# Kernel optimization log

Measured on AMD Instinct MI355X. Metric: run time of the kernel, lower is better.

## Reference

```python
import jax, jax.numpy as jnp
import numpy as np
from jax import lax

# Problem sizes (match input_specs)
N, D, M = 16384, 1024, 128
# GaussBAE hyperparameters: scl (init 1.0), alpha=sparse_reg, beta=tree_reg, temp
SCL, ALPHA, BETA, TEMP = 1.0, 0.1, 1.0, 0.5


def setup_inputs() -> dict:
    key = jax.random.key(0)
    k1, k2, k3 = jax.random.split(key, 3)
    X = jax.random.normal(k1, (N, D), jnp.float32)
    W = jax.random.normal(k2, (D, M), jnp.float32) / np.float32(np.sqrt(D))
    S0 = jax.random.randint(k3, (N, M), 0, 2).astype(jnp.int32)  # binary init states
    b = jnp.zeros((D,), jnp.float32)
    return {"X": X, "S0": S0, "W": W, "b": b}


def gibbs_sweep(X, S0, W):
    """Faithful JAX port of update_concepts_asym_cntr (one sweep, steps=1).

    Sequential over samples i (outer scan) and features j (inner scan),
    with rank-1 running updates of StS = S^T S and St1 = S^T 1.
    Deterministic ascending i/j order (original uses random permutations);
    Bernoulli uniforms are pre-drawn with a fixed key.
    """
    n, m = S0.shape
    S = S0.astype(jnp.float32)
    C = X @ W                                        # (n, m): X[i] @ W[:, j]
    U = jax.random.uniform(jax.random.key(1), (n, m), jnp.float32)
    StS = S.T @ S                                    # (m, m)
    St1 = S.sum(0)                                   # (m,)
    nf = jnp.float32(n)

    def outer_step(carry, xs):
        St1, StS = carry
        s_i, c_i, u_i = xs                           # (m,), (m,), (m,)
        # remove sample i from running stats
        St1 = St1 - s_i
        StS = StS - jnp.outer(s_i, s_i)
        # 2x2 contingency counts for each concept pair (m, m)
        D1 = StS
        D2 = St1[None, :] - StS
        D3 = St1[:, None] - StS
        D4 = nf - 1.0 - St1[None, :] - St1[:, None] + StS
        b1 = ((D1 < D2) & (D1 < D3) & (D1 < D4)).astype(jnp.float32)
        b2 = ((D2 < D1) & (D2 < D3) & (D2 < D4)).astype(jnp.float32)
        b3 = ((D3 < D2) & (D3 < D1) & (D3 < D4)).astype(jnp.float32)
        b4 = ((D4 < D2) & (D4 < D3) & (D4 < D1)).astype(jnp.float32)
        R = b1 - b2 - b3 + b4                        # (m, m)
        r = b2.sum(0) - b4.sum(0)                    # (m,)
        # centered input drive (constant over inner loop)
        inp = 2.0 * c_i - SCL * (nf - 1.0 - 2.0 * St1) / nf - ALPHA

        def inner_step(s, j):
            # tree-regularizer inhibition depends on current (partially updated) s
            inhib = R[j] @ s + r[j]
            prob = jax.nn.sigmoid((inp[j] - BETA * SCL * inhib) / TEMP)
            s = s.at[j].set((u_i[j] < prob).astype(jnp.float32))
            return s, None

        s_new, _ = lax.scan(inner_step, s_i, jnp.arange(m))
        # add updated sample i back to running stats
        St1 = St1 + s_new
        StS = StS + jnp.outer(s_new, s_new)
        return (St1, StS), s_new

    (_, _), S_new = lax.scan(outer_step, (St1, StS), (S, C, U))
    return S_new                                     # (n, m) in {0, 1}


def reference(X, S0, W, b):
    S_new = gibbs_sweep(X, S0, W)
    # GaussBAE.__call__: scl * S @ W.T + b
    out = SCL * (S_new @ W.T) + b
    return out
```

## Files before the change

### kernel.cpp

```cpp
#include <hip/hip_runtime.h>
#include <cmath>

typedef unsigned long long u64;
typedef unsigned int u32;

#define N_SAMP 16384
#define M_C 128

#define DEFER_ROW0 10240
#define DEFER_ROWS 192

__device__ __forceinline__ void tf2x32(u32 x0, u32 x1, u32& o0, u32& o1) {
  const u32 k0 = 0u, k1 = 1u;
  const u32 ks2 = k0 ^ k1 ^ 0x1BD11BDAu;
  x0 += k0; x1 += k1;
#define RND(r) { x0 += x1; x1 = (x1 << (r)) | (x1 >> (32 - (r))); x1 ^= x0; }
  RND(13) RND(15) RND(26) RND(6)  x0 += k1;  x1 += ks2 + 1u;
  RND(17) RND(29) RND(16) RND(24) x0 += ks2; x1 += k0 + 2u;
  RND(13) RND(15) RND(26) RND(6)  x0 += k0;  x1 += k1 + 3u;
  RND(17) RND(29) RND(16) RND(24) x0 += k1;  x1 += ks2 + 4u;
  RND(13) RND(15) RND(26) RND(6)  x0 += ks2; x1 += k0 + 5u;
#undef RND
  o0 = x0; o1 = x1;
}

__global__ void k_logit(float* __restrict__ Ub, double* __restrict__ Lgb) {
  int tid = blockIdx.x * 256 + threadIdx.x;
  if (tid >= N_SAMP * M_C) return;
  u32 o0, o1; tf2x32(0u, (u32)tid, o0, o1);
  u32 bits = o0 ^ o1;
  float u = __uint_as_float((bits >> 9) | 0x3f800000u) - 1.0f;
  Ub[tid] = u;
  double lg;
  if (u <= 0.0f) lg = -1e300;
  else { double ud = (double)u; lg = 0.5 * (log(ud) - log1p(-ud)); }
  Lgb[tid] = lg;
}

__global__ void k_pack(const int* __restrict__ S0, u64* __restrict__ S0m) {
  int row = blockIdx.x; int lane = threadIdx.x;
  int v0 = S0[row * 128 + lane];
  int v1 = S0[row * 128 + 64 + lane];
  u64 lo = __ballot(v0 != 0);
  u64 hi = __ballot(v1 != 0);
  if (lane == 0) { S0m[row * 2] = lo; S0m[row * 2 + 1] = hi; }
}

__global__ void k_colbits(const u64* __restrict__ S0m, u64* __restrict__ colb) {
  int wblk = blockIdx.x; int lane = threadIdx.x;
  int row = wblk * 64 + lane;
  u64 lo = S0m[row * 2], hi = S0m[row * 2 + 1];
  for (int cc = 0; cc < 64; ++cc) {
    u64 bal = __ballot((int)((lo >> cc) & 1ull));
    if (lane == 0) colb[cc * 256 + wblk] = bal;
  }
  for (int cc = 0; cc < 64; ++cc) {
    u64 bal = __ballot((int)((hi >> cc) & 1ull));
    if (lane == 0) colb[(64 + cc) * 256 + wblk] = bal;
  }
}

__global__ __launch_bounds__(256) void k_sts(const u64* __restrict__ colb, int* __restrict__ StSg) {
  int tid = blockIdx.x * 256 + threadIdx.x;
  int c = tid >> 7, k = tid & 127;
  int s = 0;
  for (int ww = 0; ww < 256; ++ww)
    s += __popcll(colb[c * 256 + ww] & colb[k * 256 + ww]);
  StSg[c * 128 + k] = s;
}

__global__ __launch_bounds__(256) void k_gemmC(const float* __restrict__ X,
                                               const float* __restrict__ W,
                                               double* __restrict__ Cb) {
  __shared__ float Xs[16][128];
  const int t = threadIdx.x;
  const int i0 = blockIdx.x * 16;
  const int j = t & 127;
  const int ih = t >> 7;
  double acc[8];
#pragma unroll
  for (int m = 0; m < 8; ++m) acc[m] = 0.0;
  for (int k0 = 0; k0 < 1024; k0 += 128) {
    __syncthreads();
#pragma unroll
    for (int m = 0; m < 8; ++m) {
      int e = t + 256 * m;
      int r = e >> 7, cc = e & 127;
      Xs[r][cc] = X[(i0 + r) * 1024 + k0 + cc];
    }
    __syncthreads();
#pragma unroll 4
    for (int kk = 0; kk < 128; ++kk) {
      double wd = (double)W[(k0 + kk) * 128 + j];
#pragma unroll
      for (int m = 0; m < 8; ++m)
        acc[m] += (double)Xs[ih * 8 + m][kk] * wd;
    }
  }
#pragma unroll
  for (int m = 0; m < 8; ++m)
    Cb[(i0 + ih * 8 + m) * 128 + j] = acc[m];
}

__global__ void k_wt(const float* __restrict__ W, float* __restrict__ Wt) {
  int d0 = blockIdx.x; int j = threadIdx.x;
  Wt[j * 1024 + d0] = W[d0 * 128 + j];
}

__device__ __forceinline__ bool condQ(double inpd, float uv, int hh) {
  double d = inpd - (double)hh;
  double pr = 1.0 / (1.0 + exp(-2.0 * d));
  return (double)uv < pr;
}

__device__ __forceinline__ int computeQ(double cv, float uv, double lg, int st1p) {
  double inp = 2.0 * cv - (16383.0 - 2.0 * (double)st1p) * (1.0 / 16384.0) - 0.1;
  if (uv <= 0.0f) return (1 << 20);
  double gd = floor(inp - lg);
  gd = fmin(fmax(gd, -300.0), 300.0);
  int h = (int)gd;
  if (condQ(inp, uv, h)) {
    if (condQ(inp, uv, h + 1)) { h++; if (condQ(inp, uv, h + 1)) h++; }
  } else {
    h--; if (!condQ(inp, uv, h)) h--;
  }
  return h;
}

__global__ __launch_bounds__(1024, 1) void k_gibbs(
    const double* __restrict__ Cb, const float* __restrict__ Ub,
    const double* __restrict__ Lgb, const u64* __restrict__ S0m,
    const int* __restrict__ StSg, u64* __restrict__ Som)
{
  __shared__ int RbufI[4096];
  __shared__ __align__(16) int St1s[128];
  __shared__ int redR[8][128];
  __shared__ int redP[8][128];
  __shared__ double cbuf[2][128];
  __shared__ float ubuf[2][128];
  __shared__ double lbuf[2][128];
  __shared__ int qbuf[128];
  __shared__ u32 simask[2][4];
  __shared__ u32 pnmask[4];
  __shared__ u32 pomask[4];

  const int t = threadIdx.x;
  const int lane = t & 63;
  const int w = t >> 6;
  const int c = t & 127;
  const int g = t >> 7;

  int sts[16];
#pragma unroll
  for (int m = 0; m < 16; ++m) sts[m] = StSg[c * 128 + g * 16 + m];

  if (t < 128) St1s[t] = StSg[t * 129];
  if (t < 4) { pnmask[t] = 0u; pomask[t] = 0u;
               simask[0][t] = (u32)(S0m[t >> 1] >> ((t & 1) * 32)); }
  if (w == 1) {
    cbuf[0][lane] = Cb[lane];            cbuf[0][64 + lane] = Cb[64 + lane];
    ubuf[0][lane] = Ub[lane];            ubuf[0][64 + lane] = Ub[64 + lane];
    lbuf[0][lane] = Lgb[lane];           lbuf[0][64 + lane] = Lgb[64 + lane];
  }
  __syncthreads();

#pragma unroll 1
  for (int i = 0; i < N_SAMP; ++i) {
    const int buf = i & 1;

    if (w == 1 && (i + 1) < N_SAMP) {
      const int nb = buf ^ 1;
      cbuf[nb][lane]      = Cb[(i + 1) * 128 + lane];
      cbuf[nb][64 + lane] = Cb[(i + 1) * 128 + 64 + lane];
      ubuf[nb][lane]      = Ub[(i + 1) * 128 + lane];
      ubuf[nb][64 + lane] = Ub[(i + 1) * 128 + 64 + lane];
      lbuf[nb][lane]      = Lgb[(i + 1) * 128 + lane];
      lbuf[nb][64 + lane] = Lgb[(i + 1) * 128 + 64 + lane];
      if (lane < 4)
        simask[nb][lane] = (u32)(S0m[(i + 1) * 2 + (lane >> 1)] >> ((lane & 1) * 32));
    }

    if (w == 2 || w == 3) {
      const int cc = t & 127;
      u32 sic = (simask[buf][cc >> 5] >> (cc & 31)) & 1u;
      int st1p = St1s[cc] - (int)sic;
      qbuf[cc] = computeQ(cbuf[buf][cc], ubuf[buf][cc], lbuf[buf][cc], st1p);
    }

    u32 PNw = (pnmask[g >> 1] >> ((g & 1) * 16)) & 0xffffu;
    u32 POw = (pomask[g >> 1] >> ((g & 1) * 16)) & 0xffffu;
    u32 SIw = (simask[buf][g >> 1] >> ((g & 1) * 16)) & 0xffffu;
    u32 pn_c = (pnmask[c >> 5] >> (c & 31)) & 1u;
    u32 po_c = (pomask[c >> 5] >> (c & 31)) & 1u;
    u32 si_c = (simask[buf][c >> 5] >> (c & 31)) & 1u;
    u32 Pw = pn_c ? PNw : 0u;
    u32 Mw = po_c ? POw : 0u;
    u32 Sw = si_c ? SIw : 0u;
    int p1 = St1s[c] - (int)si_c;
    int cpq = 16383 - p1;
    int racc = 0, pacc = 0;
#pragma unroll
    for (int ch = 0; ch < 4; ++ch) {
      int4 q4 = *(const int4*)&St1s[g * 16 + ch * 4];
      int qarr[4] = { q4.x, q4.y, q4.z, q4.w };
      u32 word = 0u;
#pragma unroll
      for (int e = 0; e < 4; ++e) {
        const int kk = ch * 4 + e;
        int a = sts[kk] + (int)((Pw >> kk) & 1u) - (int)((Mw >> kk) & 1u);
        sts[kk] = a;
        int sik = (int)((SIw >> kk) & 1u);
        int ap = a - (int)((Sw >> kk) & 1u);
        int q = qarr[e] - sik;
        int D2 = q - ap, D3 = p1 - ap, D4 = cpq - q + ap;
        int m14 = min(ap, D4), m23 = min(D2, D3);
        bool A = m14 < m23, B = m23 < m14;
        int R = (A && (ap != D4)) ? 1 : ((B && (D2 != D3)) ? -1 : 0);
        int b24 = (int)(B && (D3 < D2)) - (int)(A && (D4 < ap));
        racc += b24;
        pacc += R * sik;
        word |= ((u32)(R & 255)) << (8 * e);
      }
      RbufI[c * 32 + ((g * 4 + ch) ^ (c & 31))] = (int)word;
    }
    redR[g][c] = racc;
    redP[g][c] = pacc;
    __syncthreads();

    if (w == 0) {
      int rlo = 0, rhi = 0, plo = 0, phi = 0;
#pragma unroll
      for (int gg = 0; gg < 8; ++gg) {
        rlo += redR[gg][lane];       rhi += redR[gg][lane + 64];
        plo += redP[gg][lane];       phi += redP[gg][lane + 64];
      }
      u64 si_lo = (u64)simask[buf][0] | ((u64)simask[buf][1] << 32);
      u64 si_hi = (u64)simask[buf][2] | ((u64)simask[buf][3] << 32);
      int qlo = qbuf[lane] - rlo;
      int qhi = qbuf[lane + 64] - rhi;
      u64 nm_lo = 0ull, nm_hi = 0ull;
      const int rowL = lane * 32;
      const int rowH = (lane + 64) * 32;
      const int sw = lane & 31;

      int tl3[3], th3[3];
      tl3[0] = RbufI[rowL + (0 ^ sw)]; th3[0] = RbufI[rowH + (0 ^ sw)];
      tl3[1] = RbufI[rowL + (1 ^ sw)]; th3[1] = RbufI[rowH + (1 ^ sw)];
      int u2a = RbufI[rowH + (16 ^ sw)];
      int u2b = RbufI[rowH + (17 ^ sw)];
#pragma unroll
      for (int dw = 0; dw < 16; ++dw) {
        const int tl = tl3[dw % 3], th = th3[dw % 3];
        if (dw < 14) {
          tl3[(dw + 2) % 3] = RbufI[rowL + ((dw + 2) ^ sw)];
          th3[(dw + 2) % 3] = RbufI[rowH + ((dw + 2) ^ sw)];
        }
#pragma unroll
        for (int e = 0; e < 4; ++e) {
          const int j = dw * 4 + e;
          u64 mk = __ballot(plo <= qlo);
          int sn = (int)((mk >> j) & 1ull);
          int dlt = sn - (int)((si_lo >> j) & 1ull);
          nm_lo |= ((u64)(u32)sn) << j;
          int cl = (tl << (24 - 8 * e)) >> 24;
          int chh = (th << (24 - 8 * e)) >> 24;
          plo += cl * dlt;
          phi += chh * dlt;
        }
      }

      int v3[3];
      v3[0] = u2a; v3[1] = u2b;
#pragma unroll
      for (int dw = 0; dw < 16; ++dw) {
        const int th = v3[dw % 3];
        if (dw < 14)
          v3[(dw + 2) % 3] = RbufI[rowH + ((16 + dw + 2) ^ sw)];
#pragma unroll
        for (int e = 0; e < 4; ++e) {
          const int j = dw * 4 + e;
          u64 mk = __ballot(phi <= qhi);
          int sn = (int)((mk >> j) & 1ull);
          int dlt = sn - (int)((si_hi >> j) & 1ull);
          nm_hi |= ((u64)(u32)sn) << j;
          int chh = (th << (24 - 8 * e)) >> 24;
          phi += chh * dlt;
        }
      }

      St1s[lane]      += (int)((nm_lo >> lane) & 1ull) - (int)((si_lo >> lane) & 1ull);
      St1s[lane + 64] += (int)((nm_hi >> lane) & 1ull) - (int)((si_hi >> lane) & 1ull);
      if (lane == 0) {
        pnmask[0] = (u32)nm_lo; pnmask[1] = (u32)(nm_lo >> 32);
        pnmask[2] = (u32)nm_hi; pnmask[3] = (u32)(nm_hi >> 32);
        pomask[0] = (u32)si_lo; pomask[1] = (u32)(si_lo >> 32);
        pomask[2] = (u32)si_hi; pomask[3] = (u32)(si_hi >> 32);
        Som[i * 2] = nm_lo; Som[i * 2 + 1] = nm_hi;
      }
    }
    __syncthreads();
  }
}

__global__ __launch_bounds__(256) void k_out1(const u64* __restrict__ Som,
                                              const float* __restrict__ Wt,
                                              const float* __restrict__ bb,
                                              float* __restrict__ out) {
  if (blockIdx.x >= (DEFER_ROW0 / 4) && blockIdx.x < ((DEFER_ROW0 + DEFER_ROWS) / 4)) return;
  const int t = threadIdx.x;
  const int i0 = blockIdx.x * 4;
  u64 ml[4], mh[4];
#pragma unroll
  for (int ii = 0; ii < 4; ++ii) { ml[ii] = Som[(i0 + ii) * 2]; mh[ii] = Som[(i0 + ii) * 2 + 1]; }
  float acc[4][4];
#pragma unroll
  for (int q = 0; q < 4; ++q) {
    float bv = bb[t + 256 * q];
#pragma unroll
    for (int ii = 0; ii < 4; ++ii) acc[ii][q] = bv;
  }
#pragma unroll 2
  for (int j = 0; j < 64; ++j) {
    float wv[4];
#pragma unroll
    for (int q = 0; q < 4; ++q) wv[q] = Wt[j * 1024 + t + 256 * q];
#pragma unroll
    for (int ii = 0; ii < 4; ++ii) {
      float sb = (float)((ml[ii] >> j) & 1ull);
#pragma unroll
      for (int q = 0; q < 4; ++q) acc[ii][q] += sb * wv[q];
    }
  }
#pragma unroll 2
  for (int j = 0; j < 64; ++j) {
    float wv[4];
#pragma unroll
    for (int q = 0; q < 4; ++q) wv[q] = Wt[(64 + j) * 1024 + t + 256 * q];
#pragma unroll
    for (int ii = 0; ii < 4; ++ii) {
      float sb = (float)((mh[ii] >> j) & 1ull);
#pragma unroll
      for (int q = 0; q < 4; ++q) acc[ii][q] += sb * wv[q];
    }
  }
#pragma unroll
  for (int ii = 0; ii < 4; ++ii)
#pragma unroll
    for (int q = 0; q < 4; ++q)
      out[(i0 + ii) * 1024 + t + 256 * q] = acc[ii][q];
}

__global__ __launch_bounds__(1024) void k_out2(const u64* __restrict__ Som,
                                               const float* __restrict__ W,
                                               const float* __restrict__ bb,
                                               float* __restrict__ out) {
  __shared__ u64 sm[DEFER_ROWS * 2];
  const int t = threadIdx.x;
  if (t < DEFER_ROWS * 2) sm[t] = Som[DEFER_ROW0 * 2 + t];
  __syncthreads();
  const float bv = bb[t];
  for (int rc = 0; rc < DEFER_ROWS / 32; ++rc) {
    float acc[32];
#pragma unroll
    for (int r = 0; r < 32; ++r) acc[r] = bv;
    for (int j = 0; j < 128; ++j) {
      float wv = W[t * 128 + j];
      const int wsel = j >> 6, sh = j & 63;
#pragma unroll
      for (int r = 0; r < 32; ++r) {
        u64 m = sm[(rc * 32 + r) * 2 + wsel];
        acc[r] += (float)((m >> sh) & 1ull) * wv;
      }
    }
#pragma unroll
    for (int r = 0; r < 32; ++r)
      out[(DEFER_ROW0 + rc * 32 + r) * 1024 + t] = acc[r];
  }
}

extern "C" void kernel_launch(void* const* d_in, const int* in_sizes, int n_in,
                              void* d_out, int out_size, void* d_ws, size_t ws_size,
                              hipStream_t stream) {
  const float* X = (const float*)d_in[0];
  const int* S0  = (const int*)d_in[1];
  const float* W = (const float*)d_in[2];
  const float* b = (const float*)d_in[3];
  float* out = (float*)d_out;

  char* base = (char*)d_out;
  double* Cb  = (double*)(base);
  double* Lgb = (double*)(base + (16u << 20));
  float*  Ub  = (float*)(base + (32u << 20));
  u64*    Som = (u64*)(base + (40u << 20));
  float*  Wt  = (float*)(base + (40u << 20) + (256u << 10));
  u64*    S0m = (u64*)(base + (40u << 20) + (768u << 10));
  u64*    colb= (u64*)(base + (40u << 20) + (1024u << 10));
  int*    StSg= (int*)(base + (40u << 20) + (1280u << 10));

  k_pack   <<<16384, 64, 0, stream>>>(S0, S0m);
  k_colbits<<<256,   64, 0, stream>>>(S0m, colb);
  k_sts    <<<64,   256, 0, stream>>>(colb, StSg);
  k_gemmC  <<<1024, 256, 0, stream>>>(X, W, Cb);
  k_logit  <<<8192, 256, 0, stream>>>(Ub, Lgb);
  k_wt     <<<1024, 128, 0, stream>>>(W, Wt);
  k_gibbs  <<<1,   1024, 0, stream>>>(Cb, Ub, Lgb, S0m, StSg, Som);
  k_out1   <<<4096, 256, 0, stream>>>(Som, Wt, b, out);
  k_out2   <<<1,   1024, 0, stream>>>(Som, W, b, out);
}
```

Baseline: 115.5 ms.

## Resolve four sequential Gibbs decisions per step via threshold ballots and sdot4

Restructures the serial inner loop of the Gibbs sweep. Each group of four features now issues seven threshold ballots up front. The small intra-group corrections are derived from R entries read with readlane, and the accumulators are updated with one packed int8 dot product instead of four scalar multiply-adds. This shortens the loop-carried dependency chain of ballot then update per feature on the single wave that runs it. It also merges the two reduction arrays into one int2 array and deepens the LDS prefetch. The cost is more ballots and branchy selection logic per group.

```diff
diff --git a/kernel.cpp b/kernel.cpp
--- a/kernel.cpp
+++ b/kernel.cpp
@@ -127,6 +127,20 @@
   return h;
 }
 
+#define SEXT8(w, e) ((int)(((w) << (24 - 8 * (e))) >> 24))
+
+__device__ __forceinline__ int dot4acc(int w, int dpk, int d0, int d1, int d2, int d3, int acc) {
+#if defined(__has_builtin)
+#if __has_builtin(__builtin_amdgcn_sdot4)
+  return __builtin_amdgcn_sdot4(w, dpk, acc, false);
+#else
+  return acc + SEXT8(w,0)*d0 + SEXT8(w,1)*d1 + SEXT8(w,2)*d2 + SEXT8(w,3)*d3;
+#endif
+#else
+  return acc + SEXT8(w,0)*d0 + SEXT8(w,1)*d1 + SEXT8(w,2)*d2 + SEXT8(w,3)*d3;
+#endif
+}
+
 __global__ __launch_bounds__(1024, 1) void k_gibbs(
     const double* __restrict__ Cb, const float* __restrict__ Ub,
     const double* __restrict__ Lgb, const u64* __restrict__ S0m,
@@ -134,8 +148,7 @@
 {
   __shared__ int RbufI[4096];
   __shared__ __align__(16) int St1s[128];
-  __shared__ int redR[8][128];
-  __shared__ int redP[8][128];
+  __shared__ int2 redRP[8][128];
   __shared__ double cbuf[2][128];
   __shared__ float ubuf[2][128];
   __shared__ double lbuf[2][128];
@@ -212,7 +225,7 @@
         int sik = (int)((SIw >> kk) & 1u);
         int ap = a - (int)((Sw >> kk) & 1u);
         int q = qarr[e] - sik;
-        int D2 = q - ap, D3 = p1 - ap, D4 = cpq - q + ap;
+        int D2 = q - ap, D3 = p1 - ap, D4 = cpq - D2;
         int m14 = min(ap, D4), m23 = min(D2, D3);
         bool A = m14 < m23, B = m23 < m14;
         int R = (A && (ap != D4)) ? 1 : ((B && (D2 != D3)) ? -1 : 0);
@@ -223,16 +236,17 @@
       }
       RbufI[c * 32 + ((g * 4 + ch) ^ (c & 31))] = (int)word;
     }
-    redR[g][c] = racc;
-    redP[g][c] = pacc;
+    redRP[g][c] = make_int2(racc, pacc);
     __syncthreads();
 
     if (w == 0) {
       int rlo = 0, rhi = 0, plo = 0, phi = 0;
 #pragma unroll
       for (int gg = 0; gg < 8; ++gg) {
-        rlo += redR[gg][lane];       rhi += redR[gg][lane + 64];
-        plo += redP[gg][lane];       phi += redP[gg][lane + 64];
+        int2 a = redRP[gg][lane];
+        int2 b = redRP[gg][lane + 64];
+        rlo += a.x; plo += a.y;
+        rhi += b.x; phi += b.y;
       }
       u64 si_lo = (u64)simask[buf][0] | ((u64)simask[buf][1] << 32);
       u64 si_hi = (u64)simask[buf][2] | ((u64)simask[buf][3] << 32);
@@ -243,49 +257,94 @@
       const int rowH = (lane + 64) * 32;
       const int sw = lane & 31;
 
-      int tl3[3], th3[3];
-      tl3[0] = RbufI[rowL + (0 ^ sw)]; th3[0] = RbufI[rowH + (0 ^ sw)];
-      tl3[1] = RbufI[rowL + (1 ^ sw)]; th3[1] = RbufI[rowH + (1 ^ sw)];
+      int tl4[4], th4[4];
+      tl4[0] = RbufI[rowL + (0 ^ sw)]; th4[0] = RbufI[rowH + (0 ^ sw)];
+      tl4[1] = RbufI[rowL + (1 ^ sw)]; th4[1] = RbufI[rowH + (1 ^ sw)];
+      tl4[2] = RbufI[rowL + (2 ^ sw)]; th4[2] = RbufI[rowH + (2 ^ sw)];
       int u2a = RbufI[rowH + (16 ^ sw)];
       int u2b = RbufI[rowH + (17 ^ sw)];
+      int u2c = RbufI[rowH + (18 ^ sw)];
 #pragma unroll
       for (int dw = 0; dw < 16; ++dw) {
-        const int tl = tl3[dw % 3], th = th3[dw % 3];
-        if (dw < 14) {
-          tl3[(dw + 2) % 3] = RbufI[rowL + ((dw + 2) ^ sw)];
-          th3[(dw + 2) % 3] = RbufI[rowH + ((dw + 2) ^ sw)];
+        const int tl = tl4[dw & 3], th = th4[dw & 3];
+        if (dw < 13) {
+          tl4[(dw + 3) & 3] = RbufI[rowL + ((dw + 3) ^ sw)];
+          th4[(dw + 3) & 3] = RbufI[rowH + ((dw + 3) ^ sw)];
         }
-#pragma unroll
-        for (int e = 0; e < 4; ++e) {
-          const int j = dw * 4 + e;
-          u64 mk = __ballot(plo <= qlo);
-          int sn = (int)((mk >> j) & 1ull);
-          int dlt = sn - (int)((si_lo >> j) & 1ull);
-          nm_lo |= ((u64)(u32)sn) << j;
-          int cl = (tl << (24 - 8 * e)) >> 24;
-          int chh = (th << (24 - 8 * e)) >> 24;
-          plo += cl * dlt;
-          phi += chh * dlt;
-        }
-      }
-
-      int v3[3];
-      v3[0] = u2a; v3[1] = u2b;
+        const int j0 = 4 * dw;
+        int w1 = __builtin_amdgcn_readlane(tl, j0 + 1);
+        int w2 = __builtin_amdgcn_readlane(tl, j0 + 2);
+        int w3 = __builtin_amdgcn_readlane(tl, j0 + 3);
+        int dvv = plo - qlo;
+        u64 Bm3 = __ballot(dvv <= -3);
+        u64 Bm2 = __ballot(dvv <= -2);
+        u64 Bm1 = __ballot(dvv <= -1);
+        u64 B0  = __ballot(dvv <= 0);
+        u64 Bp1 = __ballot(dvv <= 1);
+        u64 Bp2 = __ballot(dvv <= 2);
+        u64 Bp3 = __ballot(dvv <= 3);
+        int s0 = (int)((B0 >> j0) & 1ull);
+        int d0 = s0 - (int)((si_lo >> j0) & 1ull);
+        int de1 = SEXT8(w1, 0) * d0;
+        u64 M1 = (de1 > 0) ? Bm1 : ((de1 < 0) ? Bp1 : B0);
+        int s1 = (int)((M1 >> (j0 + 1)) & 1ull);
+        int d1 = s1 - (int)((si_lo >> (j0 + 1)) & 1ull);
+        int de2 = SEXT8(w2, 0) * d0 + SEXT8(w2, 1) * d1;
+        u64 M2 = (de2 == 0) ? B0
+               : ((de2 == 1) ? Bm1 : ((de2 == -1) ? Bp1 : ((de2 == 2) ? Bm2 : Bp2)));
+        int s2 = (int)((M2 >> (j0 + 2)) & 1ull);
+        int d2 = s2 - (int)((si_lo >> (j0 + 2)) & 1ull);
+        int de3 = SEXT8(w3, 0) * d0 + SEXT8(w3, 1) * d1 + SEXT8(w3, 2) * d2;
+        u64 M3 = (de3 == 0) ? B0
+               : ((de3 == 1) ? Bm1 : ((de3 == -1) ? Bp1
+               : ((de3 == 2) ? Bm2 : ((de3 == -2) ? Bp2 : ((de3 == 3) ? Bm3 : Bp3)))));
+        int s3 = (int)((M3 >> (j0 + 3)) & 1ull);
+        int d3 = s3 - (int)((si_lo >> (j0 + 3)) & 1ull);
+        nm_lo |= ((u64)(u32)(s0 | (s1 << 1) | (s2 << 2) | (s3 << 3))) << j0;
+        int dpk = (d0 & 255) | ((d1 & 255) << 8) | ((d2 & 255) << 16) | (d3 << 24);
+        plo = dot4acc(tl, dpk, d0, d1, d2, d3, plo);
+        phi = dot4acc(th, dpk, d0, d1, d2, d3, phi);
+      }
+
+      int v4[4];
+      v4[0] = u2a; v4[1] = u2b; v4[2] = u2c;
 #pragma unroll
       for (int dw = 0; dw < 16; ++dw) {
-        const int th = v3[dw % 3];
-        if (dw < 14)
-          v3[(dw + 2) % 3] = RbufI[rowH + ((16 + dw + 2) ^ sw)];
-#pragma unroll
-        for (int e = 0; e < 4; ++e) {
-          const int j = dw * 4 + e;
-          u64 mk = __ballot(phi <= qhi);
-          int sn = (int)((mk >> j) & 1ull);
-          int dlt = sn - (int)((si_hi >> j) & 1ull);
-          nm_hi |= ((u64)(u32)sn) << j;
-          int chh = (th << (24 - 8 * e)) >> 24;
-          phi += chh * dlt;
-        }
+        const int th = v4[dw & 3];
+        if (dw < 13)
+          v4[(dw + 3) & 3] = RbufI[rowH + ((16 + dw + 3) ^ sw)];
+        const int j0 = 4 * dw;
+        int w1 = __builtin_amdgcn_readlane(th, j0 + 1);
+        int w2 = __builtin_amdgcn_readlane(th, j0 + 2);
+        int w3 = __builtin_amdgcn_readlane(th, j0 + 3);
+        int dvv = phi - qhi;
+        u64 Bm3 = __ballot(dvv <= -3);
+        u64 Bm2 = __ballot(dvv <= -2);
+        u64 Bm1 = __ballot(dvv <= -1);
+        u64 B0  = __ballot(dvv <= 0);
+        u64 Bp1 = __ballot(dvv <= 1);
+        u64 Bp2 = __ballot(dvv <= 2);
+        u64 Bp3 = __ballot(dvv <= 3);
+        int s0 = (int)((B0 >> j0) & 1ull);
+        int d0 = s0 - (int)((si_hi >> j0) & 1ull);
+        int de1 = SEXT8(w1, 0) * d0;
+        u64 M1 = (de1 > 0) ? Bm1 : ((de1 < 0) ? Bp1 : B0);
+        int s1 = (int)((M1 >> (j0 + 1)) & 1ull);
+        int d1 = s1 - (int)((si_hi >> (j0 + 1)) & 1ull);
+        int de2 = SEXT8(w2, 0) * d0 + SEXT8(w2, 1) * d1;
+        u64 M2 = (de2 == 0) ? B0
+               : ((de2 == 1) ? Bm1 : ((de2 == -1) ? Bp1 : ((de2 == 2) ? Bm2 : Bp2)));
+        int s2 = (int)((M2 >> (j0 + 2)) & 1ull);
+        int d2 = s2 - (int)((si_hi >> (j0 + 2)) & 1ull);
+        int de3 = SEXT8(w3, 0) * d0 + SEXT8(w3, 1) * d1 + SEXT8(w3, 2) * d2;
+        u64 M3 = (de3 == 0) ? B0
+               : ((de3 == 1) ? Bm1 : ((de3 == -1) ? Bp1
+               : ((de3 == 2) ? Bm2 : ((de3 == -2) ? Bp2 : ((de3 == 3) ? Bm3 : Bp3)))));
+        int s3 = (int)((M3 >> (j0 + 3)) & 1ull);
+        int d3 = s3 - (int)((si_hi >> (j0 + 3)) & 1ull);
+        nm_hi |= ((u64)(u32)(s0 | (s1 << 1) | (s2 << 2) | (s3 << 3))) << j0;
+        int dpk = (d0 & 255) | ((d1 & 255) << 8) | ((d2 & 255) << 16) | (d3 << 24);
+        phi = dot4acc(th, dpk, d0, d1, d2, d3, phi);
       }
 
       St1s[lane]      += (int)((nm_lo >> lane) & 1ull) - (int)((si_lo >> lane) & 1ull);
```

Result: slower. 230.3 ms (+99.4%).
